# Kernel tuning notes

Measured on AMD Instinct MI355X. Metric: run time of the kernel, lower is better.

The kernel has to match this reference:

```python
import jax, jax.numpy as jnp
import numpy as np

T = 32            # timesteps
DT = 1e-3
TAU_MEM_INV = 100.0   # norse LIFParameters / LIParameters default (1/1e-2)
TAU_SYN_INV = 200.0   # default (1/5e-3)
V_TH = 1.0
ALPHA = 100.0         # superspike surrogate slope

@jax.custom_vjp
def heaviside(x):
    return (x > 0).astype(x.dtype)

def _h_fwd(x):
    return heaviside(x), x

def _h_bwd(x, g):
    # superspike surrogate gradient
    return (g / (ALPHA * jnp.abs(x) + 1.0) ** 2,)

heaviside.defvjp(_h_fwd, _h_bwd)

LAYER_SIZES = [(2000, 12000), (1500, 2000), (1000, 1500), (500, 1000), (100, 500), (10, 100)]

def setup_inputs() -> dict:
    key = jax.random.key(0)
    ks = jax.random.split(key, 7)
    B = 128
    images = jax.random.normal(ks[0], (B, 3, 40, 100), dtype=jnp.float32)
    inp = {"images": images}
    for i, (out_f, in_f) in enumerate(LAYER_SIZES):
        scale = float(np.sqrt(2.0 / in_f))
        inp[f"w{i}"] = jax.random.normal(ks[i + 1], (out_f, in_f), dtype=jnp.float32) * scale
    return inp

def _encode(x):
    # norse ConstantCurrentLIFEncoder / lif_current_encode: voltage-only LIF
    def step(v, _):
        v = v + DT * TAU_MEM_INV * (-v + x)
        z = heaviside(v - V_TH)
        v = v - z * v  # v_reset = 0
        return v, z
    _, spikes = jax.lax.scan(step, jnp.zeros_like(x), None, length=T)
    return spikes  # [T, B, F]

def _lif_step(state, inp):
    # norse lif_feed_forward_step (parameter-free LIFCell)
    v, i = state
    v_dec = v + DT * TAU_MEM_INV * (-v + i)
    i_dec = i * (1.0 - DT * TAU_SYN_INV)
    z = heaviside(v_dec - V_TH)
    v_new = (1.0 - z) * v_dec  # v_reset = 0
    return (v_new, i_dec + inp), z

def _li_step(state, inp, w):
    # norse LILinearCell li_step (no bias)
    v, i = state
    i_jump = i + inp @ w.T
    v_new = v + DT * TAU_MEM_INV * (-v + i_jump)
    i_new = i_jump * (1.0 - DT * TAU_SYN_INV)
    return (v_new, i_new), v_new

def _forward(images, ws):
    B = images.shape[0]
    x = images.reshape(B, -1)  # [B, F]
    spikes = _encode(x)        # [T, B, F]
    lif_dims = [x.shape[1]] + [s[0] for s in LAYER_SIZES[:-1]]
    init_lif = tuple((jnp.zeros((B, d), x.dtype), jnp.zeros((B, d), x.dtype)) for d in lif_dims)
    init_li = tuple((jnp.zeros((B, s[0]), x.dtype), jnp.zeros((B, s[0]), x.dtype)) for s in LAYER_SIZES)

    def step(carry, s):
        lifs, lis = carry
        z = s
        new_lifs, new_lis = [], []
        for k in range(6):
            st, z = _lif_step(lifs[k], z)
            new_lifs.append(st)
            st2, z = _li_step(lis[k], z, ws[k])
            new_lis.append(st2)
        return (tuple(new_lifs), tuple(new_lis)), z

    _, outs = jax.lax.scan(step, (init_lif, init_li), spikes)  # [T, B, 10]
    out = jnp.max(outs, axis=0)
    return jax.nn.log_softmax(out, axis=1)

def reference(images, w0, w1, w2, w3, w4, w5):
    return _forward(images, (w0, w1, w2, w3, w4, w5))
```

## Files before the change

kernel.cpp:

```cpp
#include <hip/hip_runtime.h>

typedef _Float16 f16;
typedef _Float16 f16x2 __attribute__((ext_vector_type(2)));
typedef _Float16 f16x4 __attribute__((ext_vector_type(4)));
typedef _Float16 f16x8 __attribute__((ext_vector_type(8)));
typedef float f32x4 __attribute__((ext_vector_type(4)));
typedef unsigned int uint;

#define KM 0.1f
#define KS 0.8f
#define AS1 __attribute__((address_space(1)))
#define AS3 __attribute__((address_space(3)))
#define EPS_LO 2.44140625e-4f
#define KCAP0 2560
#define ASTR ((size_t)512 * KCAP0)
#define BSTR ((size_t)4096 * KCAP0)

__global__ void zero_flags(uint* __restrict__ dst, int n) {
  int i = blockIdx.x * 256 + threadIdx.x;
  if (i < n) dst[i] = 0u;
}

__global__ void enc_flags(const float* __restrict__ img, uint* __restrict__ Z,
                          uint* __restrict__ flags) {
  int idx = blockIdx.x * 256 + threadIdx.x;
  if (idx >= 128 * 3000) return;
  int b = idx / 3000, f = (idx - b * 3000) << 2;
  float4 t4 = *(const float4*)&img[b * 12000 + f];
  float x[4] = {t4.x, t4.y, t4.z, t4.w};
  float ve[4] = {0.f, 0.f, 0.f, 0.f}, vl[4] = {0.f, 0.f, 0.f, 0.f}, il[4] = {0.f, 0.f, 0.f, 0.f};
  uint m[4] = {0u, 0u, 0u, 0u};
  for (int t = 0; t < 32; ++t) {
#pragma unroll
    for (int e = 0; e < 4; ++e) {
      ve[e] = ve[e] + KM * (x[e] - ve[e]);
      float z0 = (ve[e] > 1.0f) ? 1.f : 0.f;
      ve[e] -= z0 * ve[e];
      float vd = vl[e] + KM * (il[e] - vl[e]);
      float id = KS * il[e];
      float z1 = (vd > 1.0f) ? 1.f : 0.f;
      m[e] |= (vd > 1.0f) ? (1u << t) : 0u;
      vl[e] = (1.f - z1) * vd;
      il[e] = id + z0;
    }
  }
  *(uint4*)&Z[b * 12032 + f] = make_uint4(m[0], m[1], m[2], m[3]);
  uint mask = 0u;
#pragma unroll
  for (int e = 0; e < 4; ++e) mask |= (m[e] ? 1u : 0u) << ((f & 31) + e);
  int lane = threadIdx.x & 63;
#pragma unroll
  for (int s = 1; s < 8; s <<= 1) mask |= (uint)__shfl_xor((int)mask, s);
  int g = b >> 4;
  if ((lane & 7) == 0 && mask) atomicOr(&flags[g * 376 + (f >> 5)], mask);
}

__global__ void scan_cols(const uint* __restrict__ flagsIn, int* __restrict__ colidxOut,
                          int* __restrict__ metaOut, int nwords, int cstride, int cap) {
  __shared__ int cnt[512];
  int g = blockIdx.x;
  const uint* flags = flagsIn + g * nwords;
  int* colidx = colidxOut + g * cstride;
  int* meta = metaOut + g * 2;
  int t = threadIdx.x;
  uint w = (t < nwords) ? flags[t] : 0u;
  cnt[t] = __popc(w);
  __syncthreads();
  for (int off = 1; off < 512; off <<= 1) {
    int v = cnt[t];
    int u = (t >= off) ? cnt[t - off] : 0;
    __syncthreads();
    cnt[t] = v + u;
    __syncthreads();
  }
  int base = cnt[t] - __popc(w);
  uint ww = w;
  int r = 0;
  while (ww) {
    int p = __ffs(ww) - 1;
    colidx[base + r] = t * 32 + p;
    ww &= ww - 1;
    ++r;
  }
  if (t == 511) {
    int K = cnt[511];
    if (K > cap) K = cap;
    meta[0] = K;
    meta[1] = (K + 63) & ~63;
  }
}

__global__ void spike_gather(const uint* __restrict__ Z, f16* __restrict__ A,
                             const int* __restrict__ colidx, const int* __restrict__ meta) {
  int g = blockIdx.y;
  int K = meta[g * 2], Kpc = meta[g * 2 + 1];
  if (Kpc == 0) return;
  const int* cidx = colidx + g * 12032;
  int jp = Kpc >> 1;
  int total = 16 * jp;
  for (int i = blockIdx.x * 256 + threadIdx.x; i < total; i += gridDim.x * 256) {
    int bl = i / jp, j = (i - bl * jp) << 1;
    int b = g * 16 + bl;
    uint m0 = (j < K) ? Z[b * 12032 + cidx[j]] : 0u;
    uint m1 = (j + 1 < K) ? Z[b * 12032 + cidx[j + 1]] : 0u;
    size_t base = g * ASTR + (size_t)(bl * 32) * Kpc + j;
    for (int t = 0; t < 32; ++t) {
      f16x2 s;
      s[0] = (f16)(float)((m0 >> t) & 1u);
      s[1] = (f16)(float)((m1 >> t) & 1u);
      *(f16x2*)&A[base + (size_t)t * Kpc] = s;
    }
  }
}

__global__ __launch_bounds__(512) void prep_w0_row(const float* __restrict__ W,
                                                   f16* __restrict__ dst,
                                                   const int* __restrict__ colidx,
                                                   const int* __restrict__ meta) {
  __shared__ float row[12032];
  int o = blockIdx.x;
  int tid = threadIdx.x;
  bool live = (o < 2000);
  if (live) {
    for (int f4 = tid * 4; f4 < 12000; f4 += 2048)
      *(float4*)&row[f4] = *(const float4*)&W[(size_t)o * 12000 + f4];
  }
  __syncthreads();
  int r2 = ((o >> 4) << 5) + (o & 15);
  for (int g = 0; g < 8; ++g) {
    int K = meta[g * 2], Kpc = meta[g * 2 + 1];
    const int* cidx = colidx + g * 12032;
    f16* dh = dst + g * BSTR + (size_t)r2 * Kpc;
    f16* dl = dst + g * BSTR + (size_t)(r2 + 16) * Kpc;
    for (int j = tid; j < Kpc; j += 512) {
      float w = (live && j < K) ? row[cidx[j]] : 0.f;
      f16 h = (f16)w;
      float hf = (float)h;
      if (__builtin_fabsf(hf) < 6.103515625e-05f) { h = (f16)0.f; hf = 0.f; }
      dh[j] = h;
      dl[j] = (f16)((w - hf) * 4096.0f);
    }
  }
}

__global__ __launch_bounds__(512) void prep_w1_row(const float* __restrict__ W,
                                                   f16* __restrict__ dst,
                                                   const int* __restrict__ colidx,
                                                   const int* __restrict__ meta) {
  __shared__ float row[2000];
  int K = meta[0], Kpc = meta[1];
  if (Kpc == 0) return;
  int o = blockIdx.x;
  int tid = threadIdx.x;
  bool live = (o < 1500);
  if (live) {
    for (int f4 = tid * 4; f4 < 2000; f4 += 2048)
      *(float4*)&row[f4] = *(const float4*)&W[(size_t)o * 2000 + f4];
  }
  __syncthreads();
  int r2 = ((o >> 4) << 5) + (o & 15);
  f16* dh = dst + (size_t)r2 * Kpc;
  f16* dl = dst + (size_t)(r2 + 16) * Kpc;
  for (int j = tid; j < Kpc; j += 512) {
    float w = (live && j < K) ? row[colidx[j]] : 0.f;
    f16 h = (f16)w;
    float hf = (float)h;
    if (__builtin_fabsf(hf) < 6.103515625e-05f) { h = (f16)0.f; hf = 0.f; }
    dh[j] = h;
    dl[j] = (f16)((w - hf) * 4096.0f);
  }
}

__global__ void gather_cols(const f16* __restrict__ src, f16* __restrict__ dst,
                            const int* __restrict__ colidx, const int* __restrict__ meta,
                            int srcW) {
  int K = meta[0], Kpc = meta[1];
  if (Kpc == 0) return;
  int row = blockIdx.x;
  const f16* s = src + (size_t)row * srcW;
  f16* d = dst + (size_t)row * Kpc;
  for (int j = threadIdx.x; j < Kpc; j += 256)
    d[j] = (j < K) ? s[colidx[j]] : (f16)0.f;
}

struct PrepArgs {
  const float* W[4];
  f16* dst[4];
  int Nr[4], Kr[4], Kp[4], Npd[4];
  int boff[5];
};

__global__ void prep_w_all(PrepArgs a) {
  int blk = blockIdx.x;
  int k = 0;
#pragma unroll
  for (int j = 0; j < 3; ++j) k += (blk >= a.boff[j + 1]) ? 1 : 0;
  int i = (blk - a.boff[k]) * 256 + threadIdx.x;
  int Kp = a.Kp[k];
  int kp4 = Kp >> 2;
  int total4 = a.Npd[k] * kp4;
  if (i >= total4) return;
  int o = i / kp4, f = (i - o * kp4) << 2;
  float w[4] = {0.f, 0.f, 0.f, 0.f};
  if (o < a.Nr[k] && f < a.Kr[k]) {
    float4 t = *(const float4*)&a.W[k][(size_t)o * a.Kr[k] + f];
    w[0] = t.x; w[1] = t.y; w[2] = t.z; w[3] = t.w;
  }
  f16x4 h4, l4;
#pragma unroll
  for (int e = 0; e < 4; ++e) {
    f16 h = (f16)w[e];
    float hf = (float)h;
    if (__builtin_fabsf(hf) < 6.103515625e-05f) { h = (f16)0.f; hf = 0.f; }
    h4[e] = h;
    l4[e] = (f16)((w[e] - hf) * 4096.0f);
  }
  int r2 = ((o >> 4) << 5) + (o & 15);
  *(f16x4*)&a.dst[k][(size_t)r2 * Kp + f] = h4;
  *(f16x4*)&a.dst[k][(size_t)(r2 + 16) * Kp + f] = l4;
}

template <int WM>
__global__ __launch_bounds__(WM * 128, 4)
void gemm_fused(const f16* __restrict__ A, const f16* __restrict__ B2,
                f16* __restrict__ Spk, float* __restrict__ Out,
                const int* __restrict__ kpcp, int KpFixed, int Np,
                uint* __restrict__ colFlags, int grouped) {
  constexpr int BM = WM * 64;
  constexpr int NT = WM * 128;
  constexpr int BI = 1024 / NT;
  __shared__ f16 smem[BM * 64 + 128 * 64];
  f16* sA = smem;
  f16* sB = smem + BM * 64;
  const int tid = threadIdx.x;
  const int lane = tid & 63;
  const int wave = tid >> 6;
  const int wr = wave >> 1;
  const int wc = wave & 1;

  const int nx = gridDim.x;
  const int flat = blockIdx.y * nx + blockIdx.x;
  const int cpx = (nx * gridDim.y) >> 3;
  const int id = (flat & 7) * cpx + (flat >> 3);
  const int m0 = (id / nx) * BM;
  const int n0 = (id % nx) * 128;

  int Kp;
  size_t aoff, boff;
  if (grouped) {
    int g = m0 >> 9;
    Kp = kpcp[g * 2 + 1];
    aoff = g * ASTR + (size_t)(m0 & 511) * Kp;
    boff = g * BSTR + (size_t)n0 * Kp;
  } else {
    Kp = kpcp ? kpcp[1] : KpFixed;
    aoff = (size_t)m0 * Kp;
    boff = (size_t)n0 * Kp;
  }

  f32x4 zero = {0.f, 0.f, 0.f, 0.f};
  f32x4 acc[4][4];
#pragma unroll
  for (int m = 0; m < 4; ++m)
#pragma unroll
    for (int n = 0; n < 4; ++n) acc[m][n] = zero;

  const f16* Abase = A + aoff;
  const f16* Bbase = B2 + boff;
  const int nkt = Kp >> 6;
  for (int kt = 0; kt < nkt; ++kt) {
    __syncthreads();
    const f16* Ab = Abase + (size_t)kt * 64;
    const f16* Bb = Bbase + (size_t)kt * 64;
#pragma unroll
    for (int j = 0; j < 4; ++j) {
      int q = j * NT + tid;
      int r = q >> 3, c = ((q & 7) ^ (r & 7)) * 8;
      __builtin_amdgcn_global_load_lds((const AS1 void*)(Ab + (size_t)r * Kp + c),
                                       (AS3 void*)(&sA[q * 8]), 16, 0, 0);
    }
#pragma unroll
    for (int j = 0; j < BI; ++j) {
      int q = j * NT + tid;
      int r = q >> 3, c = ((q & 7) ^ (r & 7)) * 8;
      __builtin_amdgcn_global_load_lds((const AS1 void*)(Bb + (size_t)r * Kp + c),
                                       (AS3 void*)(&sB[q * 8]), 16, 0, 0);
    }
    __syncthreads();
#pragma unroll
    for (int kk = 0; kk < 2; ++kk) {
      const int lr = lane & 15;
      const int hq = lane >> 4;
      f16x8 af[4], bf[4];
#pragma unroll
      for (int m = 0; m < 4; ++m) {
        int R = wr * 64 + m * 16 + lr;
        int ch = (kk * 4 + hq) ^ (R & 7);
        af[m] = *(const f16x8*)&sA[R * 64 + ch * 8];
      }
#pragma unroll
      for (int n = 0; n < 4; ++n) {
        int R = wc * 64 + n * 16 + lr;
        int ch = (kk * 4 + hq) ^ (R & 7);
        bf[n] = *(const f16x8*)&sB[R * 64 + ch * 8];
      }
#pragma unroll
      for (int m = 0; m < 4; ++m)
#pragma unroll
        for (int n = 0; n < 4; ++n)
          acc[m][n] = __builtin_amdgcn_mfma_f32_16x16x32_f16(af[m], bf[n], acc[m][n], 0, 0, 0);
    }
  }

  const int lr = lane & 15, lq = lane >> 4;
  float* scr = (float*)smem + wave * 1152;
  const int baseRow = m0 + wr * 64;

  if (Out) {
    __syncthreads();
#pragma unroll
    for (int m = 0; m < 4; ++m)
#pragma unroll
      for (int i = 0; i < 4; ++i)
        scr[(m * 16 + lq * 4 + i) * 17 + lr] = acc[m][0][i] + EPS_LO * acc[m][1][i];
    __syncthreads();
    float mx = -3.4e38f;
    if (lane < 32) {
      int bl = lane >> 4, c = lane & 15;
      float vL = 0.f, iL = 0.f;
      for (int t = 0; t < 32; ++t) {
        float g = scr[(bl * 32 + t) * 17 + c];
        float ij = iL + g;
        vL = vL + KM * (ij - vL);
        iL = KS * ij;
        mx = fmaxf(mx, vL);
      }
    }
    float v = (lane < 32 && (lane & 15) < 10) ? mx : -3.4e38f;
    float M = v;
#pragma unroll
    for (int s = 1; s < 16; s <<= 1) M = fmaxf(M, __shfl_xor(M, s));
    float e = (lane < 32 && (lane & 15) < 10) ? expf(v - M) : 0.f;
    float sum = e;
#pragma unroll
    for (int s = 1; s < 16; s <<= 1) sum += __shfl_xor(sum, s);
    if (n0 == 0 && wc == 0 && lane < 32 && (lane & 15) < 10) {
      int b = (baseRow >> 5) + (lane >> 4);
      Out[b * 10 + (lane & 15)] = v - M - logf(sum);
    }
    return;
  }

  __syncthreads();
#pragma unroll
  for (int h = 0; h < 2; ++h) {
#pragma unroll
    for (int m = 0; m < 4; ++m)
#pragma unroll
      for (int i = 0; i < 4; ++i)
        scr[(m * 16 + lq * 4 + i) * 17 + lr] = acc[m][2 * h][i] + EPS_LO * acc[m][2 * h + 1][i];
    __syncthreads();
    if (lane < 32) {
      int bl = lane >> 4, c = lane & 15;
      float vL = 0.f, iL = 0.f, vF = 0.f, iF = 0.f;
      for (int t = 0; t < 32; ++t) {
        float g = scr[(bl * 32 + t) * 17 + c];
        float ij = iL + g;
        vL = vL + KM * (ij - vL);
        iL = KS * ij;
        float vd = vF + KM * (iF - vF);
        float idec = KS * iF;
        float z = (vd > 1.0f) ? 1.f : 0.f;
        vF = (1.f - z) * vd;
        iF = idec + vL;
        scr[(bl * 32 + t) * 17 + c] = z;
      }
    }
    __syncthreads();
    {
      int row = lane;
      f16x8 v0, v1;
#pragma unroll
      for (int cc = 0; cc < 8; ++cc) {
        v0[cc] = (f16)scr[row * 17 + cc];
        v1[cc] = (f16)scr[row * 17 + 8 + cc];
      }
      size_t go = (size_t)(baseRow + row) * Np + (n0 >> 1) + wc * 32 + h * 16;
      *(f16x8*)&Spk[go] = v0;
      *(f16x8*)&Spk[go + 8] = v1;
      if (colFlags) {
        uint bits = 0u;
#pragma unroll
        for (int cc = 0; cc < 8; ++cc) {
          bits |= (__any((float)v0[cc] != 0.f) ? 1u : 0u) << cc;
          bits |= (__any((float)v1[cc] != 0.f) ? 1u : 0u) << (8 + cc);
        }
        int cstart = (n0 >> 1) + wc * 32 + h * 16;
        if (lane == 0 && bits) atomicOr(&colFlags[cstart >> 5], bits << (cstart & 31));
      }
    }
    __syncthreads();
  }
}

extern "C" void kernel_launch(void* const* d_in, const int* in_sizes, int n_in,
                              void* d_out, int out_size, void* d_ws, size_t ws_size,
                              hipStream_t stream) {
  const float* img = (const float*)d_in[0];
  static const int Nr[6]  = {2000, 1500, 1000, 500, 100, 10};
  static const int Kr[6]  = {12000, 2000, 1500, 1000, 500, 100};
  static const int Npd[6] = {2048, 1536, 1024, 512, 128, 128};
  static const int Kpd[6] = {12032, 2048, 1536, 1024, 512, 128};

  char* p = (char*)d_ws;
  f16* W0g = (f16*)p; p += 8 * BSTR * 2;
  f16* wa[6];
  wa[0] = W0g;
  for (int k = 1; k < 6; ++k) {
    wa[k] = (f16*)p; p += (size_t)2 * Npd[k] * Kpd[k] * 2;
  }
  f16* Ag = (f16*)p;   p += 8 * ASTR * 2;
  f16* T0 = (f16*)p;   p += (size_t)4096 * 2048 * 2;
  f16* T1 = (f16*)p;   p += (size_t)4096 * 2048 * 2;
  uint* Z = (uint*)p;  p += (size_t)128 * 12032 * 4;
  uint* flags = (uint*)p;  p += 8 * 376 * 4;
  uint* flags1 = (uint*)p; p += 64 * 4;
  int* colidx = (int*)p;  p += 8 * 12032 * 4;
  int* colidx1 = (int*)p; p += 2048 * 4;
  int* meta = (int*)p;  p += 16 * 4;
  int* meta1 = (int*)p; p += 2 * 4;

  zero_flags<<<13, 256, 0, stream>>>(flags, 8 * 376 + 64);
  enc_flags<<<(128 * 3000 + 255) / 256, 256, 0, stream>>>(img, Z, flags);
  scan_cols<<<8, 512, 0, stream>>>(flags, colidx, meta, 376, 12032, KCAP0);
  spike_gather<<<dim3(80, 8), 256, 0, stream>>>(Z, Ag, colidx, meta);
  prep_w0_row<<<2048, 512, 0, stream>>>((const float*)d_in[1], W0g, colidx, meta);

  PrepArgs pa;
  int nb = 0;
  for (int k = 2; k < 6; ++k) {
    int kk = k - 2;
    pa.W[kk] = (const float*)d_in[k + 1];
    pa.dst[kk] = wa[k];
    pa.Nr[kk] = Nr[k]; pa.Kr[kk] = Kr[k]; pa.Kp[kk] = Kpd[k]; pa.Npd[kk] = Npd[k];
    pa.boff[kk] = nb;
    nb += ((Npd[k] * Kpd[k]) >> 2) / 256;
  }
  pa.boff[4] = nb;
  prep_w_all<<<nb, 256, 0, stream>>>(pa);

  gemm_fused<4><<<dim3(32, 16), dim3(512), 0, stream>>>(
      Ag, W0g, T0, nullptr, meta, 0, Npd[0], flags1, 1);

  scan_cols<<<1, 512, 0, stream>>>(flags1, colidx1, meta1, 64, 2048, 2048);
  gather_cols<<<4096, 256, 0, stream>>>(T0, T1, colidx1, meta1, Npd[0]);
  prep_w1_row<<<1536, 512, 0, stream>>>((const float*)d_in[2], wa[1], colidx1, meta1);

  gemm_fused<4><<<dim3(2 * Npd[1] / 128, 16), dim3(512), 0, stream>>>(
      T1, wa[1], T0, nullptr, meta1, 0, Npd[1], nullptr, 0);
  gemm_fused<2><<<dim3(2 * Npd[2] / 128, 32), dim3(256), 0, stream>>>(
      T0, wa[2], T1, nullptr, nullptr, Kpd[2], Npd[2], nullptr, 0);
  gemm_fused<2><<<dim3(2 * Npd[3] / 128, 32), dim3(256), 0, stream>>>(
      T1, wa[3], T0, nullptr, nullptr, Kpd[3], Npd[3], nullptr, 0);
  gemm_fused<2><<<dim3(2 * Npd[4] / 128, 32), dim3(256), 0, stream>>>(
      T0, wa[4], T1, nullptr, nullptr, Kpd[4], Npd[4], nullptr, 0);
  gemm_fused<2><<<dim3(2 * Npd[5] / 128, 32), dim3(256), 0, stream>>>(
      T1, wa[5], nullptr, (float*)d_out, nullptr, Kpd[5], Npd[5], nullptr, 0);
}
```

Before: 172.5 us.

## Extend per-group active-column compaction to layers one and two

Column activity flags are now tracked per batch group of 512 rows for the layer-1 output and also collected for the layer-2 output. Layers 1 and 2 then gather only the columns that are active within each group and prepare matching group-specific weight copies. The goal is to skip GEMM work on all-zero spike columns in those layers. In exchange it adds scan, gather and per-group weight-prep launches, plus eight weight copies for W1 and W2. Group capacities are fixed (KCAP1 2048, KCAP2 1024), and the W2 cap holds fewer than the 1500 input columns, so a group with more than 1024 active columns would not fit.

```diff
diff --git a/kernel.cpp b/kernel.cpp
--- a/kernel.cpp
+++ b/kernel.cpp
@@ -13,8 +13,8 @@
 #define AS3 __attribute__((address_space(3)))
 #define EPS_LO 2.44140625e-4f
 #define KCAP0 2560
-#define ASTR ((size_t)512 * KCAP0)
-#define BSTR ((size_t)4096 * KCAP0)
+#define KCAP1 2048
+#define KCAP2 1024
 
 __global__ void zero_flags(uint* __restrict__ dst, int n) {
   int i = blockIdx.x * 256 + threadIdx.x;
@@ -103,7 +103,7 @@
     int b = g * 16 + bl;
     uint m0 = (j < K) ? Z[b * 12032 + cidx[j]] : 0u;
     uint m1 = (j + 1 < K) ? Z[b * 12032 + cidx[j + 1]] : 0u;
-    size_t base = g * ASTR + (size_t)(bl * 32) * Kpc + j;
+    size_t base = g * ((size_t)512 * KCAP0) + (size_t)(bl * 32) * Kpc + j;
     for (int t = 0; t < 32; ++t) {
       f16x2 s;
       s[0] = (f16)(float)((m0 >> t) & 1u);
@@ -113,27 +113,33 @@
   }
 }
 
-__global__ __launch_bounds__(512) void prep_w0_row(const float* __restrict__ W,
+template <int LROW>
+__global__ __launch_bounds__(512) void prep_wk_row(const float* __restrict__ W,
                                                    f16* __restrict__ dst,
                                                    const int* __restrict__ colidx,
-                                                   const int* __restrict__ meta) {
-  __shared__ float row[12032];
+                                                   const int* __restrict__ meta,
+                                                   int Nr, int Kr, int cstride, size_t bstr) {
+  __shared__ float row[LROW];
   int o = blockIdx.x;
   int tid = threadIdx.x;
-  bool live = (o < 2000);
+  bool live = (o < Nr);
   if (live) {
-    for (int f4 = tid * 4; f4 < 12000; f4 += 2048)
-      *(float4*)&row[f4] = *(const float4*)&W[(size_t)o * 12000 + f4];
+    for (int f4 = tid * 4; f4 < Kr; f4 += 2048)
+      *(float4*)&row[f4] = *(const float4*)&W[(size_t)o * Kr + f4];
   }
   __syncthreads();
   int r2 = ((o >> 4) << 5) + (o & 15);
   for (int g = 0; g < 8; ++g) {
     int K = meta[g * 2], Kpc = meta[g * 2 + 1];
-    const int* cidx = colidx + g * 12032;
-    f16* dh = dst + g * BSTR + (size_t)r2 * Kpc;
-    f16* dl = dst + g * BSTR + (size_t)(r2 + 16) * Kpc;
+    const int* cidx = colidx + g * cstride;
+    f16* dh = dst + g * bstr + (size_t)r2 * Kpc;
+    f16* dl = dst + g * bstr + (size_t)(r2 + 16) * Kpc;
     for (int j = tid; j < Kpc; j += 512) {
-      float w = (live && j < K) ? row[cidx[j]] : 0.f;
+      float w = 0.f;
+      if (live && j < K) {
+        int c = cidx[j];
+        w = (c < Kr) ? row[c] : 0.f;
+      }
       f16 h = (f16)w;
       float hf = (float)h;
       if (__builtin_fabsf(hf) < 6.103515625e-05f) { h = (f16)0.f; hf = 0.f; }
@@ -143,44 +149,18 @@
   }
 }
 
-__global__ __launch_bounds__(512) void prep_w1_row(const float* __restrict__ W,
-                                                   f16* __restrict__ dst,
-                                                   const int* __restrict__ colidx,
-                                                   const int* __restrict__ meta) {
-  __shared__ float row[2000];
-  int K = meta[0], Kpc = meta[1];
-  if (Kpc == 0) return;
-  int o = blockIdx.x;
-  int tid = threadIdx.x;
-  bool live = (o < 1500);
-  if (live) {
-    for (int f4 = tid * 4; f4 < 2000; f4 += 2048)
-      *(float4*)&row[f4] = *(const float4*)&W[(size_t)o * 2000 + f4];
-  }
-  __syncthreads();
-  int r2 = ((o >> 4) << 5) + (o & 15);
-  f16* dh = dst + (size_t)r2 * Kpc;
-  f16* dl = dst + (size_t)(r2 + 16) * Kpc;
-  for (int j = tid; j < Kpc; j += 512) {
-    float w = (live && j < K) ? row[colidx[j]] : 0.f;
-    f16 h = (f16)w;
-    float hf = (float)h;
-    if (__builtin_fabsf(hf) < 6.103515625e-05f) { h = (f16)0.f; hf = 0.f; }
-    dh[j] = h;
-    dl[j] = (f16)((w - hf) * 4096.0f);
-  }
-}
-
 __global__ void gather_cols(const f16* __restrict__ src, f16* __restrict__ dst,
                             const int* __restrict__ colidx, const int* __restrict__ meta,
-                            int srcW) {
-  int K = meta[0], Kpc = meta[1];
+                            int srcW, int cstride, size_t astr) {
+  int row = blockIdx.x;
+  int g = row >> 9;
+  int K = meta[g * 2], Kpc = meta[g * 2 + 1];
   if (Kpc == 0) return;
-  int row = blockIdx.x;
+  const int* cidx = colidx + g * cstride;
   const f16* s = src + (size_t)row * srcW;
-  f16* d = dst + (size_t)row * Kpc;
+  f16* d = dst + g * astr + (size_t)(row & 511) * Kpc;
   for (int j = threadIdx.x; j < Kpc; j += 256)
-    d[j] = (j < K) ? s[colidx[j]] : (f16)0.f;
+    d[j] = (j < K) ? s[cidx[j]] : (f16)0.f;
 }
 
 struct PrepArgs {
@@ -225,7 +205,8 @@
 void gemm_fused(const f16* __restrict__ A, const f16* __restrict__ B2,
                 f16* __restrict__ Spk, float* __restrict__ Out,
                 const int* __restrict__ kpcp, int KpFixed, int Np,
-                uint* __restrict__ colFlags, int grouped) {
+                uint* __restrict__ colFlags, int cfw, int grouped,
+                size_t astr, size_t bstr) {
   constexpr int BM = WM * 64;
   constexpr int NT = WM * 128;
   constexpr int BI = 1024 / NT;
@@ -250,8 +231,8 @@
   if (grouped) {
     int g = m0 >> 9;
     Kp = kpcp[g * 2 + 1];
-    aoff = g * ASTR + (size_t)(m0 & 511) * Kp;
-    boff = g * BSTR + (size_t)n0 * Kp;
+    aoff = g * astr + (size_t)(m0 & 511) * Kp;
+    boff = g * bstr + (size_t)n0 * Kp;
   } else {
     Kp = kpcp ? kpcp[1] : KpFixed;
     aoff = (size_t)m0 * Kp;
@@ -396,7 +377,9 @@
           bits |= (__any((float)v1[cc] != 0.f) ? 1u : 0u) << (8 + cc);
         }
         int cstart = (n0 >> 1) + wc * 32 + h * 16;
-        if (lane == 0 && bits) atomicOr(&colFlags[cstart >> 5], bits << (cstart & 31));
+        int g1 = baseRow >> 9;
+        if (lane == 0 && bits)
+          atomicOr(&colFlags[g1 * cfw + (cstart >> 5)], bits << (cstart & 31));
       }
     }
     __syncthreads();
@@ -407,63 +390,79 @@
                               void* d_out, int out_size, void* d_ws, size_t ws_size,
                               hipStream_t stream) {
   const float* img = (const float*)d_in[0];
-  static const int Nr[6]  = {2000, 1500, 1000, 500, 100, 10};
-  static const int Kr[6]  = {12000, 2000, 1500, 1000, 500, 100};
-  static const int Npd[6] = {2048, 1536, 1024, 512, 128, 128};
-  static const int Kpd[6] = {12032, 2048, 1536, 1024, 512, 128};
 
   char* p = (char*)d_ws;
-  f16* W0g = (f16*)p; p += 8 * BSTR * 2;
-  f16* wa[6];
-  wa[0] = W0g;
-  for (int k = 1; k < 6; ++k) {
-    wa[k] = (f16*)p; p += (size_t)2 * Npd[k] * Kpd[k] * 2;
-  }
-  f16* Ag = (f16*)p;   p += 8 * ASTR * 2;
-  f16* T0 = (f16*)p;   p += (size_t)4096 * 2048 * 2;
-  f16* T1 = (f16*)p;   p += (size_t)4096 * 2048 * 2;
-  uint* Z = (uint*)p;  p += (size_t)128 * 12032 * 4;
+  f16* W0g = (f16*)p; p += 8 * (size_t)4096 * KCAP0 * 2;
+  f16* W1g = (f16*)p; p += 8 * (size_t)3072 * KCAP1 * 2;
+  f16* W2g = (f16*)p; p += 8 * (size_t)2048 * KCAP2 * 2;
+  f16* W3 = (f16*)p;  p += (size_t)2 * 512 * 1024 * 2;
+  f16* W4 = (f16*)p;  p += (size_t)2 * 128 * 512 * 2;
+  f16* W5 = (f16*)p;  p += (size_t)2 * 128 * 128 * 2;
+  f16* Ag = (f16*)p;  p += 8 * (size_t)512 * KCAP0 * 2;
+  f16* T0 = (f16*)p;  p += (size_t)4096 * 2048 * 2;
+  f16* T1 = (f16*)p;  p += (size_t)4096 * 2048 * 2;
+  uint* Z = (uint*)p; p += (size_t)128 * 12032 * 4;
   uint* flags = (uint*)p;  p += 8 * 376 * 4;
-  uint* flags1 = (uint*)p; p += 64 * 4;
+  uint* flags1 = (uint*)p; p += 8 * 64 * 4;
+  uint* flags2 = (uint*)p; p += 8 * 48 * 4;
   int* colidx = (int*)p;  p += 8 * 12032 * 4;
-  int* colidx1 = (int*)p; p += 2048 * 4;
+  int* colidx1 = (int*)p; p += 8 * 2048 * 4;
+  int* colidx2 = (int*)p; p += 8 * 1536 * 4;
   int* meta = (int*)p;  p += 16 * 4;
-  int* meta1 = (int*)p; p += 2 * 4;
-
-  zero_flags<<<13, 256, 0, stream>>>(flags, 8 * 376 + 64);
+  int* meta1 = (int*)p; p += 16 * 4;
+  int* meta2 = (int*)p; p += 16 * 4;
+
+  zero_flags<<<16, 256, 0, stream>>>(flags, 8 * 376 + 8 * 64 + 8 * 48);
   enc_flags<<<(128 * 3000 + 255) / 256, 256, 0, stream>>>(img, Z, flags);
   scan_cols<<<8, 512, 0, stream>>>(flags, colidx, meta, 376, 12032, KCAP0);
   spike_gather<<<dim3(80, 8), 256, 0, stream>>>(Z, Ag, colidx, meta);
-  prep_w0_row<<<2048, 512, 0, stream>>>((const float*)d_in[1], W0g, colidx, meta);
+  prep_wk_row<12032><<<2048, 512, 0, stream>>>((const float*)d_in[1], W0g, colidx, meta,
+                                               2000, 12000, 12032, (size_t)4096 * KCAP0);
 
   PrepArgs pa;
+  static const int Nr3[3] = {500, 100, 10}, Kr3[3] = {1000, 500, 100};
+  static const int Kp3[3] = {1024, 512, 128}, Np3[3] = {512, 128, 128};
+  f16* dst3[3] = {W3, W4, W5};
   int nb = 0;
-  for (int k = 2; k < 6; ++k) {
-    int kk = k - 2;
-    pa.W[kk] = (const float*)d_in[k + 1];
-    pa.dst[kk] = wa[k];
-    pa.Nr[kk] = Nr[k]; pa.Kr[kk] = Kr[k]; pa.Kp[kk] = Kpd[k]; pa.Npd[kk] = Npd[k];
-    pa.boff[kk] = nb;
-    nb += ((Npd[k] * Kpd[k]) >> 2) / 256;
-  }
+  for (int k = 0; k < 3; ++k) {
+    pa.W[k] = (const float*)d_in[k + 4];
+    pa.dst[k] = dst3[k];
+    pa.Nr[k] = Nr3[k]; pa.Kr[k] = Kr3[k]; pa.Kp[k] = Kp3[k]; pa.Npd[k] = Np3[k];
+    pa.boff[k] = nb;
+    nb += ((Np3[k] * Kp3[k]) >> 2) / 256;
+  }
+  pa.boff[3] = nb;
   pa.boff[4] = nb;
   prep_w_all<<<nb, 256, 0, stream>>>(pa);
 
   gemm_fused<4><<<dim3(32, 16), dim3(512), 0, stream>>>(
-      Ag, W0g, T0, nullptr, meta, 0, Npd[0], flags1, 1);
-
-  scan_cols<<<1, 512, 0, stream>>>(flags1, colidx1, meta1, 64, 2048, 2048);
-  gather_cols<<<4096, 256, 0, stream>>>(T0, T1, colidx1, meta1, Npd[0]);
-  prep_w1_row<<<1536, 512, 0, stream>>>((const float*)d_in[2], wa[1], colidx1, meta1);
-
-  gemm_fused<4><<<dim3(2 * Npd[1] / 128, 16), dim3(512), 0, stream>>>(
-      T1, wa[1], T0, nullptr, meta1, 0, Npd[1], nullptr, 0);
-  gemm_fused<2><<<dim3(2 * Npd[2] / 128, 32), dim3(256), 0, stream>>>(
-      T0, wa[2], T1, nullptr, nullptr, Kpd[2], Npd[2], nullptr, 0);
-  gemm_fused<2><<<dim3(2 * Npd[3] / 128, 32), dim3(256), 0, stream>>>(
-      T1, wa[3], T0, nullptr, nullptr, Kpd[3], Npd[3], nullptr, 0);
-  gemm_fused<2><<<dim3(2 * Npd[4] / 128, 32), dim3(256), 0, stream>>>(
-      T0, wa[4], T1, nullptr, nullptr, Kpd[4], Npd[4], nullptr, 0);
-  gemm_fused<2><<<dim3(2 * Npd[5] / 128, 32), dim3(256), 0, stream>>>(
-      T1, wa[5], nullptr, (float*)d_out, nullptr, Kpd[5], Npd[5], nullptr, 0);
-}
+      Ag, W0g, T0, nullptr, meta, 0, 2048, flags1, 64, 1,
+      (size_t)512 * KCAP0, (size_t)4096 * KCAP0);
+
+  scan_cols<<<8, 512, 0, stream>>>(flags1, colidx1, meta1, 64, 2048, KCAP1);
+  gather_cols<<<4096, 256, 0, stream>>>(T0, T1, colidx1, meta1, 2048, 2048,
+                                        (size_t)512 * KCAP1);
+  prep_wk_row<2048><<<1536, 512, 0, stream>>>((const float*)d_in[2], W1g, colidx1, meta1,
+                                              1500, 2000, 2048, (size_t)3072 * KCAP1);
+
+  gemm_fused<4><<<dim3(24, 16), dim3(512), 0, stream>>>(
+      T1, W1g, T0, nullptr, meta1, 0, 1536, flags2, 48, 1,
+      (size_t)512 * KCAP1, (size_t)3072 * KCAP1);
+
+  scan_cols<<<8, 512, 0, stream>>>(flags2, colidx2, meta2, 48, 1536, KCAP2);
+  gather_cols<<<4096, 256, 0, stream>>>(T0, T1, colidx2, meta2, 1536, 1536,
+                                        (size_t)512 * KCAP2);
+  prep_wk_row<1536><<<1024, 512, 0, stream>>>((const float*)d_in[3], W2g, colidx2, meta2,
+                                              1000, 1500, 1536, (size_t)2048 * KCAP2);
+
+  gemm_fused<2><<<dim3(16, 32), dim3(256), 0, stream>>>(
+      T1, W2g, T0, nullptr, meta2, 0, 1024, nullptr, 0, 1,
+      (size_t)512 * KCAP2, (size_t)2048 * KCAP2);
+
+  gemm_fused<2><<<dim3(8, 32), dim3(256), 0, stream>>>(
+      T0, W3, T1, nullptr, nullptr, 1024, 512, nullptr, 0, 0, 0, 0);
+  gemm_fused<2><<<dim3(2, 32), dim3(256), 0, stream>>>(
+      T1, W4, T0, nullptr, nullptr, 512, 128, nullptr, 0, 0, 0, 0);
+  gemm_fused<2><<<dim3(2, 32), dim3(256), 0, stream>>>(
+      T0, W5, nullptr, (float*)d_out, nullptr, 128, 128, nullptr, 0, 0, 0, 0);
+}
```

Result: faster. 158.3 us (-8.2%).
